# Kernel optimization log

Hardware: AMD Instinct MI355X
Metric: run time of the kernel (lower is better)

Reference implementation:

```python
import jax, jax.numpy as jnp
import numpy as np

B, S, D, H, F, L = 8, 1024, 512, 8, 2048, 2
SLOTS, OUT = 512, 32
NEG = jnp.finfo(jnp.float32).min


def _ln(x, scale, bias, eps=1e-6):
    mu = jnp.mean(x, axis=-1, keepdims=True)
    var = jnp.var(x, axis=-1, keepdims=True)
    return (x - mu) * jax.lax.rsqrt(var + eps) * scale + bias


def _mha(q_in, kv_in, Wq, Wk, Wv, Wo, mask):
    # flax MultiHeadDotProductAttention, use_bias=False; query scaled by 1/sqrt(head_dim)
    hd = D // H
    b = q_in.shape[0]
    q = (q_in @ Wq).reshape(b, -1, H, hd) / jnp.sqrt(jnp.float32(hd))
    k = (kv_in @ Wk).reshape(b, -1, H, hd)
    v = (kv_in @ Wv).reshape(b, -1, H, hd)
    scores = jnp.einsum('bqhd,bkhd->bhqk', q, k)
    scores = jnp.where(mask, scores, NEG)
    w = jax.nn.softmax(scores, axis=-1)
    o = jnp.einsum('bhqk,bkhd->bqhd', w, v).reshape(b, -1, D)
    return o @ Wo


def _forward(s, x, t, Wq, Wk, Wv, Wo, cWq, cWk, cWv, cWo, ln1_s, ln1_b, ln2_s, ln2_b, ln3_s, ln3_b, W1, b1, W2, b2, lnf_s, lnf_b, Wout, bout, W_vs, b_vs, W_ss, b_ss):
    causal = jnp.tril(jnp.ones((S, S), dtype=bool))[None, None]  # [1,1,S,S]
    eye = jnp.eye(S, dtype=bool)[None, None]                     # [1,1,S,S]
    dec = s
    for l in range(L):
        dec = _ln(dec + _mha(dec, dec, Wq[l], Wk[l], Wv[l], Wo[l], causal), ln1_s[l], ln1_b[l])
        dec = _ln(dec + _mha(dec, t, cWq[l], cWk[l], cWv[l], cWo[l], eye), ln2_s[l], ln2_b[l])
        ff = jax.nn.relu(dec @ W1[l] + b1[l]) @ W2[l] + b2[l]
        dec = _ln(dec + ff, ln3_s[l], ln3_b[l])
    logits = _ln(dec, lnf_s, lnf_b) @ Wout + bout  # [B,S,D]
    keys = jax.nn.softmax(logits.reshape(-1, logits.shape[-1]), axis=1)  # [N,D]
    Vs = (keys @ W_vs + b_vs).reshape(-1, SLOTS, OUT)  # [N,slots,out]
    Ss = keys @ W_ss + b_ss                            # [N,slots]
    xf = x.reshape(-1, OUT)                            # [N,out]
    denom = jnp.linalg.norm(Vs, axis=2) * jnp.linalg.norm(xf, axis=1, keepdims=True)  # [N,slots]
    scores = jnp.einsum('nko,no->nk', Vs, xf) / denom
    idx = jnp.argmax(scores, axis=1)  # [N]
    s_out = jnp.take_along_axis(Ss, idx[:, None], axis=1).reshape(-1, S)            # [B,S]
    v_out = jnp.take_along_axis(Vs, idx[:, None, None], axis=1).reshape(-1, S, OUT)  # [B,S,out]
    return v_out, s_out, Ss


def setup_inputs():
    key = jax.random.key(0)
    ks = iter(jax.random.split(key, 32))
    def r(shape, sc=0.02):
        return jax.random.normal(next(ks), shape, jnp.float32) * sc
    return {
        's': jax.random.normal(next(ks), (B, S, D), jnp.float32),
        'x': jax.random.normal(next(ks), (B, S, OUT), jnp.float32),
        't': jax.random.normal(next(ks), (B, S, D), jnp.float32),
        'Wq': r((L, D, D)), 'Wk': r((L, D, D)), 'Wv': r((L, D, D)), 'Wo': r((L, D, D)),
        'cWq': r((L, D, D)), 'cWk': r((L, D, D)), 'cWv': r((L, D, D)), 'cWo': r((L, D, D)),
        'ln1_s': jnp.ones((L, D)), 'ln1_b': jnp.zeros((L, D)),
        'ln2_s': jnp.ones((L, D)), 'ln2_b': jnp.zeros((L, D)),
        'ln3_s': jnp.ones((L, D)), 'ln3_b': jnp.zeros((L, D)),
        'W1': r((L, D, F)), 'b1': jnp.zeros((L, F)),
        'W2': r((L, F, D)), 'b2': jnp.zeros((L, D)),
        'lnf_s': jnp.ones((D,)), 'lnf_b': jnp.zeros((D,)),
        'Wout': r((D, D)), 'bout': jnp.zeros((D,)),
        'W_vs': r((D, SLOTS * OUT)), 'b_vs': jnp.zeros((SLOTS * OUT,)),
        'W_ss': r((D, SLOTS)), 'b_ss': jnp.zeros((SLOTS,)),
    }


def reference(s, x, t, Wq, Wk, Wv, Wo, cWq, cWk, cWv, cWo, ln1_s, ln1_b, ln2_s, ln2_b, ln3_s, ln3_b, W1, b1, W2, b2, lnf_s, lnf_b, Wout, bout, W_vs, b_vs, W_ss, b_ss):
    return _forward(s, x, t, Wq, Wk, Wv, Wo, cWq, cWk, cWv, cWo, ln1_s, ln1_b, ln2_s, ln2_b, ln3_s, ln3_b, W1, b1, W2, b2, lnf_s, lnf_b, Wout, bout, W_vs, b_vs, W_ss, b_ss)
```

## Files before the change

### kernel.cpp

```cpp
#include <hip/hip_runtime.h>
#include <math.h>

namespace {
constexpr int kD   = 512;
constexpr int kN   = 8192;
constexpr int kS   = 1024;
constexpr int kHD  = 64;
constexpr int kFF  = 2048;
constexpr int kSL  = 512;
constexpr int kOUT = 32;
}

typedef __bf16 bf16x8 __attribute__((ext_vector_type(8)));
typedef float  f32x4  __attribute__((ext_vector_type(4)));

__device__ inline unsigned short f2bf(float x) {
    unsigned u = __float_as_uint(x);
    return (unsigned short)((u + 0x7FFF + ((u >> 16) & 1)) >> 16);
}
__device__ inline void split2(float x, unsigned short& h, unsigned short& l) {
    unsigned u = __float_as_uint(x);
    unsigned hb = (u + 0x7FFF + ((u >> 16) & 1)) >> 16;
    h = (unsigned short)hb;
    float hf = __uint_as_float(hb << 16);
    l = f2bf(x - hf);
}

template<int MODE, int RELU, int HAS_BIAS>
__global__ __launch_bounds__(256)
void mgemm_k(const unsigned short* __restrict__ Ah, const unsigned short* __restrict__ Al,
             const unsigned short* __restrict__ Bh, const unsigned short* __restrict__ Bl,
             const float* __restrict__ bias, float* __restrict__ C,
             unsigned short* __restrict__ Ch, unsigned short* __restrict__ Cl,
             const float* __restrict__ X, const float* __restrict__ XN,
             float* __restrict__ SC,
             int M, int N, int K, float alpha)
{
    __shared__ uint4 smem_u4[4096];
    unsigned char* smem = (unsigned char*)smem_u4;
    const int tid  = threadIdx.x;
    const int lane = tid & 63;
    const int w    = tid >> 6;
    const int brow = blockIdx.y * 128;
    const int bcol = blockIdx.x * 128;
    const int wr = (w >> 1) * 64, wc = (w & 1) * 64;
    const size_t Kb = (size_t)K * 2;

    const unsigned short* srcM; int rb;
    if      (w == 0) { srcM = Ah; rb = brow; }
    else if (w == 1) { srcM = Al; rb = brow; }
    else if (w == 2) { srcM = Bh; rb = bcol; }
    else             { srcM = Bl; rb = bcol; }
    const int swzsrc = (((lane & 7) << 4) ^ (((lane >> 3) & 7) << 4));
    const unsigned char* srow = (const unsigned char*)srcM
                              + (size_t)(rb + (lane >> 3)) * Kb + swzsrc;
    unsigned char* dbase = smem + w * 16384;

    const int lm = lane & 15;
    const int lg = lane >> 4;
    const int lswz = (lane & 7);

    f32x4 acc[4][4];
#pragma unroll
    for (int i = 0; i < 4; ++i)
#pragma unroll
        for (int j = 0; j < 4; ++j) acc[i][j] = (f32x4)(0.f);

    for (int k0 = 0; k0 < K; k0 += 64) {
#pragma unroll
        for (int j = 0; j < 16; ++j) {
            const unsigned char* sp = srow + (size_t)(j * 8) * Kb + (size_t)k0 * 2;
            __builtin_amdgcn_global_load_lds(
                (const __attribute__((address_space(1))) unsigned int*)sp,
                (__attribute__((address_space(3))) unsigned int*)(dbase + j * 1024),
                16, 0, 0);
        }
        __syncthreads();
#pragma unroll
        for (int ks = 0; ks < 2; ++ks) {
            const int kf = (((ks << 2) + lg) ^ lswz) << 4;
            bf16x8 bh[4], bl[4];
#pragma unroll
            for (int n = 0; n < 4; ++n) {
                const int r = wc + n * 16 + lm;
                bh[n] = *(const bf16x8*)(smem + 32768 + r * 128 + kf);
                bl[n] = *(const bf16x8*)(smem + 49152 + r * 128 + kf);
            }
#pragma unroll
            for (int m = 0; m < 4; ++m) {
                const int r = wr + m * 16 + lm;
                bf16x8 ah = *(const bf16x8*)(smem +         r * 128 + kf);
                bf16x8 al = *(const bf16x8*)(smem + 16384 + r * 128 + kf);
#pragma unroll
                for (int n = 0; n < 4; ++n) {
                    acc[m][n] = __builtin_amdgcn_mfma_f32_16x16x32_bf16(al, bh[n], acc[m][n], 0, 0, 0);
                    acc[m][n] = __builtin_amdgcn_mfma_f32_16x16x32_bf16(ah, bl[n], acc[m][n], 0, 0, 0);
                    acc[m][n] = __builtin_amdgcn_mfma_f32_16x16x32_bf16(ah, bh[n], acc[m][n], 0, 0, 0);
                }
            }
        }
        __syncthreads();
    }

    if (MODE == 0 || MODE == 1) {
#pragma unroll
        for (int n = 0; n < 4; ++n) {
            const int colg = bcol + wc + n * 16 + lm;
            const float bv = HAS_BIAS ? bias[colg] : 0.f;
#pragma unroll
            for (int m = 0; m < 4; ++m) {
                const int rowb = brow + wr + m * 16 + lg * 4;
#pragma unroll
                for (int r = 0; r < 4; ++r) {
                    float v = alpha * acc[m][n][r] + bv;
                    if (RELU) v = fmaxf(v, 0.f);
                    if (MODE == 0) {
                        C[(size_t)(rowb + r) * N + colg] = v;
                    } else {
                        unsigned short h, l;
                        split2(v, h, l);
                        Ch[(size_t)(rowb + r) * N + colg] = h;
                        Cl[(size_t)(rowb + r) * N + colg] = l;
                    }
                }
            }
        }
    } else {
        float bv[4];
#pragma unroll
        for (int n = 0; n < 4; ++n) bv[n] = bias[bcol + wc + n * 16 + lm];
        const int slot0 = (bcol + wc) >> 5;
#pragma unroll
        for (int m = 0; m < 4; ++m) {
#pragma unroll
            for (int r = 0; r < 4; ++r) {
                const int row = brow + wr + m * 16 + lg * 4 + r;
                const float x0 = X[(size_t)row * kOUT + lm];
                const float x1 = X[(size_t)row * kOUT + 16 + lm];
                const float xn = XN[row];
#pragma unroll
                for (int s = 0; s < 2; ++s) {
                    const float v0 = acc[m][2 * s][r]     + bv[2 * s];
                    const float v1 = acc[m][2 * s + 1][r] + bv[2 * s + 1];
                    float pd = v0 * x0 + v1 * x1;
                    float pn = v0 * v0 + v1 * v1;
                    pd += __shfl_xor(pd, 1); pd += __shfl_xor(pd, 2);
                    pd += __shfl_xor(pd, 4); pd += __shfl_xor(pd, 8);
                    pn += __shfl_xor(pn, 1); pn += __shfl_xor(pn, 2);
                    pn += __shfl_xor(pn, 4); pn += __shfl_xor(pn, 8);
                    if (lm == 0)
                        SC[(size_t)row * kSL + slot0 + s] = pd / (sqrtf(pn) * xn);
                }
            }
        }
    }
}

__global__ __launch_bounds__(256)
void tsplit_k(const float* __restrict__ W, unsigned short* __restrict__ TH,
              unsigned short* __restrict__ TL, int K, int N)
{
    __shared__ float t[32][33];
    const int tid = threadIdx.x;
    const int n0 = blockIdx.x * 32, k0 = blockIdx.y * 32;
    {
        const int r = tid >> 3, c = (tid & 7) * 4;
        const float4 v = *(const float4*)(W + (size_t)(k0 + r) * N + n0 + c);
        t[r][c] = v.x; t[r][c + 1] = v.y; t[r][c + 2] = v.z; t[r][c + 3] = v.w;
    }
    __syncthreads();
    const int rn = tid >> 3, ck = (tid & 7) * 4;
    unsigned short h[4], l[4];
#pragma unroll
    for (int i = 0; i < 4; ++i) split2(t[ck + i][rn], h[i], l[i]);
    *(ushort4*)(TH + (size_t)(n0 + rn) * K + k0 + ck) = make_ushort4(h[0], h[1], h[2], h[3]);
    *(ushort4*)(TL + (size_t)(n0 + rn) * K + k0 + ck) = make_ushort4(l[0], l[1], l[2], l[3]);
}

__global__ __launch_bounds__(256)
void split_k(const float* __restrict__ in, unsigned short* __restrict__ hi,
             unsigned short* __restrict__ lo, int n4)
{
    int i = blockIdx.x * 256 + threadIdx.x;
    const int stride = gridDim.x * 256;
    for (; i < n4; i += stride) {
        const float4 v = *(const float4*)(in + (size_t)i * 4);
        unsigned short h[4], l[4];
        split2(v.x, h[0], l[0]); split2(v.y, h[1], l[1]);
        split2(v.z, h[2], l[2]); split2(v.w, h[3], l[3]);
        *(ushort4*)(hi + (size_t)i * 4) = make_ushort4(h[0], h[1], h[2], h[3]);
        *(ushort4*)(lo + (size_t)i * 4) = make_ushort4(l[0], l[1], l[2], l[3]);
    }
}

__global__ __launch_bounds__(256)
void attn_k(const float* __restrict__ Q, const float* __restrict__ K,
            const float* __restrict__ V, float* __restrict__ O)
{
    __shared__ float Qs[64][68];
    __shared__ float Ks[64][68];
    __shared__ float Vs[64][68];
    __shared__ float Ps[64][68];
    const int tid = threadIdx.x;
    const int tr = tid >> 4, tc = tid & 15;
    const int qt = blockIdx.x & 15;
    const int h  = (blockIdx.x >> 4) & 7;
    const int b  = blockIdx.x >> 7;
    const int q0 = qt * 64;
    const float* Qb = Q + ((size_t)(b * kS + q0)) * kD + h * kHD;
    {
        const int r = tid >> 2;
#pragma unroll
        for (int it = 0; it < 4; ++it) {
            const int e0 = ((tid & 3) << 2) + it * 16;
            const float4 q4 = *(const float4*)(Qb + (size_t)r * kD + e0);
            Qs[e0 + 0][r] = q4.x; Qs[e0 + 1][r] = q4.y;
            Qs[e0 + 2][r] = q4.z; Qs[e0 + 3][r] = q4.w;
        }
    }
    float m[4], l[4], acc[4][4];
#pragma unroll
    for (int i = 0; i < 4; ++i) {
        m[i] = -INFINITY; l[i] = 0.f;
#pragma unroll
        for (int j = 0; j < 4; ++j) acc[i][j] = 0.f;
    }
    for (int j0 = 0; j0 <= q0; j0 += 64) {
        const float* Kb = K + ((size_t)(b * kS + j0)) * kD + h * kHD;
        const float* Vb = V + ((size_t)(b * kS + j0)) * kD + h * kHD;
        __syncthreads();
        {
            const int c = tid >> 2;
#pragma unroll
            for (int it = 0; it < 4; ++it) {
                const int e0 = ((tid & 3) << 2) + it * 16;
                const float4 k4 = *(const float4*)(Kb + (size_t)c * kD + e0);
                Ks[e0 + 0][c] = k4.x; Ks[e0 + 1][c] = k4.y;
                Ks[e0 + 2][c] = k4.z; Ks[e0 + 3][c] = k4.w;
                *(float4*)&Vs[c][e0] = *(const float4*)(Vb + (size_t)c * kD + e0);
            }
        }
        __syncthreads();
        float s[4][4];
#pragma unroll
        for (int i = 0; i < 4; ++i)
#pragma unroll
            for (int j = 0; j < 4; ++j) s[i][j] = 0.f;
        for (int e = 0; e < 64; ++e) {
            float qa[4], kb[4];
            *(float4*)&qa[0] = *(const float4*)&Qs[e][tr * 4];
            *(float4*)&kb[0] = *(const float4*)&Ks[e][tc * 4];
#pragma unroll
            for (int i = 0; i < 4; ++i)
#pragma unroll
                for (int j = 0; j < 4; ++j)
                    s[i][j] = fmaf(qa[i], kb[j], s[i][j]);
        }
        if (j0 == q0) {
#pragma unroll
            for (int i = 0; i < 4; ++i)
#pragma unroll
                for (int j = 0; j < 4; ++j)
                    if (tc * 4 + j > tr * 4 + i) s[i][j] = -INFINITY;
        }
#pragma unroll
        for (int i = 0; i < 4; ++i) {
            float rm = fmaxf(fmaxf(s[i][0], s[i][1]), fmaxf(s[i][2], s[i][3]));
            rm = fmaxf(rm, __shfl_xor(rm, 1));
            rm = fmaxf(rm, __shfl_xor(rm, 2));
            rm = fmaxf(rm, __shfl_xor(rm, 4));
            rm = fmaxf(rm, __shfl_xor(rm, 8));
            const float mn = fmaxf(m[i], rm);
            const float co = expf(m[i] - mn);
            float ps = 0.f;
#pragma unroll
            for (int j = 0; j < 4; ++j) { s[i][j] = expf(s[i][j] - mn); ps += s[i][j]; }
            ps += __shfl_xor(ps, 1); ps += __shfl_xor(ps, 2);
            ps += __shfl_xor(ps, 4); ps += __shfl_xor(ps, 8);
            l[i] = l[i] * co + ps;
            m[i] = mn;
#pragma unroll
            for (int j = 0; j < 4; ++j) acc[i][j] *= co;
            *(float4*)&Ps[tr * 4 + i][tc * 4] = make_float4(s[i][0], s[i][1], s[i][2], s[i][3]);
        }
        __syncthreads();
        for (int c = 0; c < 64; ++c) {
            const float4 v4 = *(const float4*)&Vs[c][tc * 4];
#pragma unroll
            for (int i = 0; i < 4; ++i) {
                const float p = Ps[tr * 4 + i][c];
                acc[i][0] = fmaf(p, v4.x, acc[i][0]);
                acc[i][1] = fmaf(p, v4.y, acc[i][1]);
                acc[i][2] = fmaf(p, v4.z, acc[i][2]);
                acc[i][3] = fmaf(p, v4.w, acc[i][3]);
            }
        }
    }
    float* Ob = O + ((size_t)(b * kS + q0)) * kD + h * kHD;
#pragma unroll
    for (int i = 0; i < 4; ++i) {
        const float inv = 1.0f / l[i];
        *(float4*)(Ob + (size_t)(tr * 4 + i) * kD + tc * 4) =
            make_float4(acc[i][0] * inv, acc[i][1] * inv, acc[i][2] * inv, acc[i][3] * inv);
    }
}

__global__ __launch_bounds__(256)
void ln_k(const float* __restrict__ a, const float* __restrict__ b,
          const float* __restrict__ sc, const float* __restrict__ bi,
          float* __restrict__ out, unsigned short* __restrict__ oh,
          unsigned short* __restrict__ ol)
{
    const int w = threadIdx.x >> 6, lane = threadIdx.x & 63;
    const size_t row = (size_t)blockIdx.x * 4 + w;
    const float* ap = a + row * kD;
    float x[8];
    *(float4*)&x[0] = *(const float4*)(ap + lane * 8);
    *(float4*)&x[4] = *(const float4*)(ap + lane * 8 + 4);
    if (b) {
        const float* bp = b + row * kD;
        float y[8];
        *(float4*)&y[0] = *(const float4*)(bp + lane * 8);
        *(float4*)&y[4] = *(const float4*)(bp + lane * 8 + 4);
#pragma unroll
        for (int k = 0; k < 8; ++k) x[k] += y[k];
    }
    float s = 0.f;
#pragma unroll
    for (int k = 0; k < 8; ++k) s += x[k];
    for (int msk = 1; msk < 64; msk <<= 1) s += __shfl_xor(s, msk);
    const float mean = s * (1.0f / 512.0f);
    float v = 0.f;
#pragma unroll
    for (int k = 0; k < 8; ++k) { const float d = x[k] - mean; v = fmaf(d, d, v); }
    for (int msk = 1; msk < 64; msk <<= 1) v += __shfl_xor(v, msk);
    const float rstd = 1.0f / sqrtf(v * (1.0f / 512.0f) + 1e-6f);
    float o[8]; unsigned short h[8], lo2[8];
#pragma unroll
    for (int k = 0; k < 8; ++k) {
        const int col = lane * 8 + k;
        o[k] = (x[k] - mean) * rstd * sc[col] + bi[col];
        split2(o[k], h[k], lo2[k]);
    }
    *(float4*)(out + row * kD + lane * 8)     = *(const float4*)&o[0];
    *(float4*)(out + row * kD + lane * 8 + 4) = *(const float4*)&o[4];
    *(ushort4*)(oh + row * kD + lane * 8)     = make_ushort4(h[0], h[1], h[2], h[3]);
    *(ushort4*)(oh + row * kD + lane * 8 + 4) = make_ushort4(h[4], h[5], h[6], h[7]);
    *(ushort4*)(ol + row * kD + lane * 8)     = make_ushort4(lo2[0], lo2[1], lo2[2], lo2[3]);
    *(ushort4*)(ol + row * kD + lane * 8 + 4) = make_ushort4(lo2[4], lo2[5], lo2[6], lo2[7]);
}

__global__ __launch_bounds__(256)
void softmax_k(const float* __restrict__ in, float* __restrict__ out,
               unsigned short* __restrict__ oh, unsigned short* __restrict__ ol)
{
    const int w = threadIdx.x >> 6, lane = threadIdx.x & 63;
    const size_t row = (size_t)blockIdx.x * 4 + w;
    const float* ip = in + row * kD;
    float x[8];
    *(float4*)&x[0] = *(const float4*)(ip + lane * 8);
    *(float4*)&x[4] = *(const float4*)(ip + lane * 8 + 4);
    float mx = x[0];
#pragma unroll
    for (int k = 1; k < 8; ++k) mx = fmaxf(mx, x[k]);
    for (int msk = 1; msk < 64; msk <<= 1) mx = fmaxf(mx, __shfl_xor(mx, msk));
    float s = 0.f;
#pragma unroll
    for (int k = 0; k < 8; ++k) { x[k] = expf(x[k] - mx); s += x[k]; }
    for (int msk = 1; msk < 64; msk <<= 1) s += __shfl_xor(s, msk);
    const float inv = 1.0f / s;
    unsigned short h[8], lo2[8];
#pragma unroll
    for (int k = 0; k < 8; ++k) { x[k] *= inv; split2(x[k], h[k], lo2[k]); }
    *(float4*)(out + row * kD + lane * 8)     = *(const float4*)&x[0];
    *(float4*)(out + row * kD + lane * 8 + 4) = *(const float4*)&x[4];
    *(ushort4*)(oh + row * kD + lane * 8)     = make_ushort4(h[0], h[1], h[2], h[3]);
    *(ushort4*)(oh + row * kD + lane * 8 + 4) = make_ushort4(h[4], h[5], h[6], h[7]);
    *(ushort4*)(ol + row * kD + lane * 8)     = make_ushort4(lo2[0], lo2[1], lo2[2], lo2[3]);
    *(ushort4*)(ol + row * kD + lane * 8 + 4) = make_ushort4(lo2[4], lo2[5], lo2[6], lo2[7]);
}

__global__ __launch_bounds__(256)
void xnorm_k(const float* __restrict__ X, float* __restrict__ XN)
{
    const int tid = threadIdx.x;
    const int row = blockIdx.x * 8 + (tid >> 5);
    const int o = tid & 31;
    const float v = X[(size_t)row * kOUT + o];
    float s = v * v;
    s += __shfl_xor(s, 1); s += __shfl_xor(s, 2); s += __shfl_xor(s, 4);
    s += __shfl_xor(s, 8); s += __shfl_xor(s, 16);
    if (o == 0) XN[row] = sqrtf(s);
}

__global__ __launch_bounds__(256)
void pick_k(const float* __restrict__ scores, const float* __restrict__ keys,
            const float* __restrict__ Wvs, const float* __restrict__ bvs,
            const float* __restrict__ Ss, float* __restrict__ vout,
            float* __restrict__ sout)
{
    const int n = blockIdx.x;
    const int tid = threadIdx.x;
    __shared__ float sv[256];
    __shared__ int   si[256];
    __shared__ float ks[512];
    __shared__ float red[256];
    const float s0 = scores[(size_t)n * kSL + tid];
    const float s1 = scores[(size_t)n * kSL + tid + 256];
    float bs; int bi;
    if (s1 > s0) { bs = s1; bi = tid + 256; } else { bs = s0; bi = tid; }
    sv[tid] = bs; si[tid] = bi;
    ks[tid] = keys[(size_t)n * kD + tid];
    ks[tid + 256] = keys[(size_t)n * kD + tid + 256];
    __syncthreads();
    for (int off = 128; off > 0; off >>= 1) {
        if (tid < off) {
            const float ov = sv[tid + off]; const int oi = si[tid + off];
            if (ov > sv[tid] || (ov == sv[tid] && oi < si[tid])) { sv[tid] = ov; si[tid] = oi; }
        }
        __syncthreads();
    }
    const int idx = si[0];
    const int o = tid & 31;
    const int seg = tid >> 5;
    const float* Wc = Wvs + (size_t)idx * kOUT + o;
    float part = 0.f;
    for (int d = seg * 64; d < seg * 64 + 64; ++d)
        part = fmaf(ks[d], Wc[(size_t)d * (kSL * kOUT)], part);
    red[tid] = part;
    __syncthreads();
    if (tid < 32) {
        float t = red[tid];
#pragma unroll
        for (int ss = 1; ss < 8; ++ss) t += red[tid + 32 * ss];
        vout[(size_t)n * kOUT + tid] = t + bvs[idx * kOUT + tid];
    }
    if (tid == 0) sout[n] = Ss[(size_t)n * kSL + idx];
}

extern "C" void kernel_launch(void* const* d_in, const int* in_sizes, int n_in,
                              void* d_out, int out_size, void* d_ws, size_t ws_size,
                              hipStream_t stream)
{
    (void)in_sizes; (void)n_in; (void)out_size; (void)ws_size;
    const float* s_in = (const float*)d_in[0];
    const float* x_in = (const float*)d_in[1];
    const float* t_in = (const float*)d_in[2];
    const float* Wq   = (const float*)d_in[3];
    const float* Wk   = (const float*)d_in[4];
    const float* Wv   = (const float*)d_in[5];
    const float* Wo   = (const float*)d_in[6];
    const float* cWv  = (const float*)d_in[9];
    const float* cWo  = (const float*)d_in[10];
    const float* ln1s = (const float*)d_in[11];
    const float* ln1b = (const float*)d_in[12];
    const float* ln2s = (const float*)d_in[13];
    const float* ln2b = (const float*)d_in[14];
    const float* ln3s = (const float*)d_in[15];
    const float* ln3b = (const float*)d_in[16];
    const float* W1   = (const float*)d_in[17];
    const float* b1   = (const float*)d_in[18];
    const float* W2   = (const float*)d_in[19];
    const float* b2   = (const float*)d_in[20];
    const float* lnfs = (const float*)d_in[21];
    const float* lnfb = (const float*)d_in[22];
    const float* Wout = (const float*)d_in[23];
    const float* bout = (const float*)d_in[24];
    const float* Wvs  = (const float*)d_in[25];
    const float* bvs  = (const float*)d_in[26];
    const float* Wss  = (const float*)d_in[27];
    const float* bss  = (const float*)d_in[28];

    float* out_v  = (float*)d_out;
    float* out_s  = out_v + (size_t)kN * kOUT;
    float* out_Ss = out_s + kN;

    unsigned char* w8 = (unsigned char*)d_ws;
    const size_t MD = (size_t)kN * kD;
    float* f_dec = (float*)w8;
    float* f_A   = f_dec + MD;
    float* f_B   = f_A + MD;
    float* f_C   = f_B + MD;
    float* f_xn  = f_C + MD;
    unsigned short* dH = (unsigned short*)(f_xn + kN);
    unsigned short* dL = dH + MD;
    unsigned short* hH = dL + MD;
    unsigned short* hL = hH + (size_t)kN * kFF;
    unsigned short* wTH = hL + (size_t)kN * kFF;
    unsigned short* wTL = wTH + (size_t)kSL * kOUT * kD;
    unsigned short* sH = hH;
    unsigned short* sL = hL;
    unsigned short* kH = hH + MD;
    unsigned short* kL = hL + MD;

    const dim3 blk(256);
    const size_t DD = (size_t)kD * kD;

    auto tsplit = [&](const float* W, int K, int N) {
        tsplit_k<<<dim3(N / 32, K / 32), blk, 0, stream>>>(W, wTH, wTL, K, N);
    };
    auto gemm = [&](const unsigned short* aH, const unsigned short* aL,
                    const float* bias, float* out, int N, int K, float alpha) {
        if (bias)
            mgemm_k<0, 0, 1><<<dim3(N / 128, kN / 128), blk, 0, stream>>>(
                aH, aL, wTH, wTL, bias, out, nullptr, nullptr, nullptr, nullptr, nullptr,
                kN, N, K, alpha);
        else
            mgemm_k<0, 0, 0><<<dim3(N / 128, kN / 128), blk, 0, stream>>>(
                aH, aL, wTH, wTL, nullptr, out, nullptr, nullptr, nullptr, nullptr, nullptr,
                kN, N, K, alpha);
    };

    xnorm_k<<<kN / 8, blk, 0, stream>>>(x_in, f_xn);
    split_k<<<1024, blk, 0, stream>>>(s_in, dH, dL, (int)(MD / 4));

    const float* cur = s_in;
    for (int l = 0; l < 2; ++l) {
        const size_t wo = (size_t)l * DD;
        tsplit(Wq + wo, kD, kD); gemm(dH, dL, nullptr, f_A, kD, kD, 0.125f);
        tsplit(Wk + wo, kD, kD); gemm(dH, dL, nullptr, f_B, kD, kD, 1.f);
        tsplit(Wv + wo, kD, kD); gemm(dH, dL, nullptr, f_C, kD, kD, 1.f);
        attn_k<<<1024, blk, 0, stream>>>(f_A, f_B, f_C, f_A);
        split_k<<<1024, blk, 0, stream>>>(f_A, sH, sL, (int)(MD / 4));
        tsplit(Wo + wo, kD, kD); gemm(sH, sL, nullptr, f_B, kD, kD, 1.f);
        ln_k<<<kN / 4, blk, 0, stream>>>(cur, f_B, ln1s + l * kD, ln1b + l * kD, f_dec, dH, dL);
        split_k<<<1024, blk, 0, stream>>>(t_in, sH, sL, (int)(MD / 4));
        tsplit(cWv + wo, kD, kD); gemm(sH, sL, nullptr, f_A, kD, kD, 1.f);
        split_k<<<1024, blk, 0, stream>>>(f_A, sH, sL, (int)(MD / 4));
        tsplit(cWo + wo, kD, kD); gemm(sH, sL, nullptr, f_A, kD, kD, 1.f);
        ln_k<<<kN / 4, blk, 0, stream>>>(f_dec, f_A, ln2s + l * kD, ln2b + l * kD, f_dec, dH, dL);
        tsplit(W1 + (size_t)l * kD * kFF, kD, kFF);
        mgemm_k<1, 1, 1><<<dim3(kFF / 128, kN / 128), blk, 0, stream>>>(
            dH, dL, wTH, wTL, b1 + (size_t)l * kFF, nullptr, hH, hL,
            nullptr, nullptr, nullptr, kN, kFF, kD, 1.f);
        tsplit(W2 + (size_t)l * kFF * kD, kFF, kD);
        gemm(hH, hL, b2 + (size_t)l * kD, f_A, kD, kFF, 1.f);
        ln_k<<<kN / 4, blk, 0, stream>>>(f_dec, f_A, ln3s + l * kD, ln3b + l * kD, f_dec, dH, dL);
        cur = f_dec;
    }
    ln_k<<<kN / 4, blk, 0, stream>>>(f_dec, nullptr, lnfs, lnfb, f_A, dH, dL);
    tsplit(Wout, kD, kD); gemm(dH, dL, bout, f_B, kD, kD, 1.f);
    softmax_k<<<kN / 4, blk, 0, stream>>>(f_B, f_A, kH, kL);
    tsplit(Wss, kD, kSL); gemm(kH, kL, bss, out_Ss, kSL, kD, 1.f);
    tsplit(Wvs, kD, kSL * kOUT);
    mgemm_k<2, 0, 1><<<dim3(kSL * kOUT / 128, kN / 128), blk, 0, stream>>>(
        kH, kL, wTH, wTL, bvs, nullptr, nullptr, nullptr, x_in, f_xn, f_C,
        kN, kSL * kOUT, kD, 1.f);
    pick_k<<<kN, blk, 0, stream>>>(f_C, f_A, Wvs, bvs, out_Ss, out_v, out_s);
}
```

Baseline: 2.190 ms.

## Add double-buffered 256x256 split-bf16 GEMM for the large FFN and slot GEMMs

Adds a new GEMM kernel with 256x256 output tiles and 512 threads. It double-buffers LDS across K-steps of 32, using async global-to-LDS loads overlapped with MFMA compute through explicit vmcnt waits. It also remaps block IDs so that nearby blocks are spread across groups of eight. The W1 FFN GEMM and the large N=16384 slot-value GEMM with the fused cosine-score epilogue use it, which should cut per-tile load traffic and hide load latency. The smaller 128-tile kernel keeps its old loop, gains the same block remap, and drops its unused epilogue arguments. The larger tiles raise register pressure and use 128KB of LDS per block, which may limit occupancy.

```diff
diff --git a/kernel.cpp b/kernel.cpp
--- a/kernel.cpp
+++ b/kernel.cpp
@@ -27,79 +27,88 @@
 }
 
 template<int MODE, int RELU, int HAS_BIAS>
-__global__ __launch_bounds__(256)
-void mgemm_k(const unsigned short* __restrict__ Ah, const unsigned short* __restrict__ Al,
-             const unsigned short* __restrict__ Bh, const unsigned short* __restrict__ Bl,
-             const float* __restrict__ bias, float* __restrict__ C,
-             unsigned short* __restrict__ Ch, unsigned short* __restrict__ Cl,
-             const float* __restrict__ X, const float* __restrict__ XN,
-             float* __restrict__ SC,
-             int M, int N, int K, float alpha)
-{
-    __shared__ uint4 smem_u4[4096];
-    unsigned char* smem = (unsigned char*)smem_u4;
-    const int tid  = threadIdx.x;
-    const int lane = tid & 63;
-    const int w    = tid >> 6;
-    const int brow = blockIdx.y * 128;
-    const int bcol = blockIdx.x * 128;
-    const int wr = (w >> 1) * 64, wc = (w & 1) * 64;
-    const size_t Kb = (size_t)K * 2;
-
-    const unsigned short* srcM; int rb;
-    if      (w == 0) { srcM = Ah; rb = brow; }
-    else if (w == 1) { srcM = Al; rb = brow; }
-    else if (w == 2) { srcM = Bh; rb = bcol; }
-    else             { srcM = Bl; rb = bcol; }
-    const int swzsrc = (((lane & 7) << 4) ^ (((lane >> 3) & 7) << 4));
-    const unsigned char* srow = (const unsigned char*)srcM
-                              + (size_t)(rb + (lane >> 3)) * Kb + swzsrc;
-    unsigned char* dbase = smem + w * 16384;
-
-    const int lm = lane & 15;
-    const int lg = lane >> 4;
-    const int lswz = (lane & 7);
-
-    f32x4 acc[4][4];
-#pragma unroll
-    for (int i = 0; i < 4; ++i)
+__global__ __launch_bounds__(512, 2)
+void mgemm256_k(const unsigned short* __restrict__ Ah, const unsigned short* __restrict__ Al,
+                const unsigned short* __restrict__ Bh, const unsigned short* __restrict__ Bl,
+                const float* __restrict__ bias, float* __restrict__ C,
+                unsigned short* __restrict__ Ch, unsigned short* __restrict__ Cl,
+                const float* __restrict__ X, const float* __restrict__ XN,
+                float* __restrict__ SC,
+                int M, int N, int K, float alpha)
+{
+    __shared__ uint4 smem4[8192];
+    unsigned char* smem = (unsigned char*)smem4;
+    const int tid = threadIdx.x, lane = tid & 63, w = tid >> 6;
+
+    const int gx = gridDim.x;
+    int bid = blockIdx.y * gx + blockIdx.x;
+    const int nwg = gx * gridDim.y;
+    bid = (bid & 7) * (nwg >> 3) + (bid >> 3);
+    const int bx = bid % gx, by = bid / gx;
+    const int brow = by * 256, bcol = bx * 256;
+    const int wr = (w >> 2) * 128, wc = (w & 3) * 64;
+    const size_t K2 = (size_t)K * 2;
+
+    const int p = w >> 1, hf = w & 1;
+    const unsigned short* SP = (p == 0) ? Ah : (p == 1) ? Al : (p == 2) ? Bh : Bl;
+    const int rbase = (p < 2) ? brow : bcol;
+    const int cch = ((lane & 3) - ((lane >> 3) & 3)) & 3;
+    const unsigned char* src0 = (const unsigned char*)SP
+        + (size_t)(rbase + hf * 128 + (lane >> 2)) * K2 + (cch << 4);
+    const int ldsw0 = (p << 14) + (hf << 13);
+
+    const int lm = lane & 15, lg = lane >> 4;
+    const int sw = ((lg + (lm >> 1)) & 3) << 4;
+    const int aoff = (wr + lm) * 64 + sw;
+    const int boff = 32768 + (wc + lm) * 64 + sw;
+
+    f32x4 acc[8][4];
+#pragma unroll
+    for (int i = 0; i < 8; ++i)
 #pragma unroll
         for (int j = 0; j < 4; ++j) acc[i][j] = (f32x4)(0.f);
 
-    for (int k0 = 0; k0 < K; k0 += 64) {
-#pragma unroll
-        for (int j = 0; j < 16; ++j) {
-            const unsigned char* sp = srow + (size_t)(j * 8) * Kb + (size_t)k0 * 2;
+    auto stage = [&](int bufo_, int t_) {
+        const unsigned char* s_ = src0 + (size_t)t_ * 64;
+#pragma unroll
+        for (int j = 0; j < 8; ++j)
             __builtin_amdgcn_global_load_lds(
-                (const __attribute__((address_space(1))) unsigned int*)sp,
-                (__attribute__((address_space(3))) unsigned int*)(dbase + j * 1024),
+                (const __attribute__((address_space(1))) unsigned int*)(s_ + (size_t)j * 16 * K2),
+                (__attribute__((address_space(3))) unsigned int*)(smem + bufo_ + ldsw0 + j * 1024),
                 16, 0, 0);
-        }
-        __syncthreads();
-#pragma unroll
-        for (int ks = 0; ks < 2; ++ks) {
-            const int kf = (((ks << 2) + lg) ^ lswz) << 4;
-            bf16x8 bh[4], bl[4];
+    };
+
+    const int nt = K >> 5;
+    stage(0, 0);
+    for (int t = 0; t < nt; ++t) {
+        if (t + 1 < nt) {
+            stage(((t + 1) & 1) << 16, t + 1);
+            asm volatile("s_waitcnt vmcnt(8)" ::: "memory");
+        } else {
+            asm volatile("s_waitcnt vmcnt(0)" ::: "memory");
+        }
+        __builtin_amdgcn_s_barrier();
+        __builtin_amdgcn_sched_barrier(0);
+        const unsigned char* base = smem + ((t & 1) << 16);
+        bf16x8 bh[4], bl[4];
+#pragma unroll
+        for (int n = 0; n < 4; ++n) {
+            bh[n] = *(const bf16x8*)(base + boff + n * 1024);
+            bl[n] = *(const bf16x8*)(base + boff + 16384 + n * 1024);
+        }
+#pragma unroll
+        for (int m = 0; m < 8; ++m) {
+            bf16x8 ah = *(const bf16x8*)(base + aoff + m * 1024);
+            bf16x8 al = *(const bf16x8*)(base + aoff + 16384 + m * 1024);
 #pragma unroll
             for (int n = 0; n < 4; ++n) {
-                const int r = wc + n * 16 + lm;
-                bh[n] = *(const bf16x8*)(smem + 32768 + r * 128 + kf);
-                bl[n] = *(const bf16x8*)(smem + 49152 + r * 128 + kf);
-            }
-#pragma unroll
-            for (int m = 0; m < 4; ++m) {
-                const int r = wr + m * 16 + lm;
-                bf16x8 ah = *(const bf16x8*)(smem +         r * 128 + kf);
-                bf16x8 al = *(const bf16x8*)(smem + 16384 + r * 128 + kf);
-#pragma unroll
-                for (int n = 0; n < 4; ++n) {
-                    acc[m][n] = __builtin_amdgcn_mfma_f32_16x16x32_bf16(al, bh[n], acc[m][n], 0, 0, 0);
-                    acc[m][n] = __builtin_amdgcn_mfma_f32_16x16x32_bf16(ah, bl[n], acc[m][n], 0, 0, 0);
-                    acc[m][n] = __builtin_amdgcn_mfma_f32_16x16x32_bf16(ah, bh[n], acc[m][n], 0, 0, 0);
-                }
-            }
-        }
-        __syncthreads();
+                acc[m][n] = __builtin_amdgcn_mfma_f32_16x16x32_bf16(al, bh[n], acc[m][n], 0, 0, 0);
+                acc[m][n] = __builtin_amdgcn_mfma_f32_16x16x32_bf16(ah, bl[n], acc[m][n], 0, 0, 0);
+                acc[m][n] = __builtin_amdgcn_mfma_f32_16x16x32_bf16(ah, bh[n], acc[m][n], 0, 0, 0);
+            }
+        }
+        __builtin_amdgcn_sched_barrier(0);
+        __builtin_amdgcn_s_barrier();
     }
 
     if (MODE == 0 || MODE == 1) {
@@ -108,7 +117,7 @@
             const int colg = bcol + wc + n * 16 + lm;
             const float bv = HAS_BIAS ? bias[colg] : 0.f;
 #pragma unroll
-            for (int m = 0; m < 4; ++m) {
+            for (int m = 0; m < 8; ++m) {
                 const int rowb = brow + wr + m * 16 + lg * 4;
 #pragma unroll
                 for (int r = 0; r < 4; ++r) {
@@ -131,7 +140,7 @@
         for (int n = 0; n < 4; ++n) bv[n] = bias[bcol + wc + n * 16 + lm];
         const int slot0 = (bcol + wc) >> 5;
 #pragma unroll
-        for (int m = 0; m < 4; ++m) {
+        for (int m = 0; m < 8; ++m) {
 #pragma unroll
             for (int r = 0; r < 4; ++r) {
                 const int row = brow + wr + m * 16 + lg * 4 + r;
@@ -150,6 +159,109 @@
                     pn += __shfl_xor(pn, 4); pn += __shfl_xor(pn, 8);
                     if (lm == 0)
                         SC[(size_t)row * kSL + slot0 + s] = pd / (sqrtf(pn) * xn);
+                }
+            }
+        }
+    }
+}
+
+template<int MODE, int RELU, int HAS_BIAS>
+__global__ __launch_bounds__(256)
+void mgemm_k(const unsigned short* __restrict__ Ah, const unsigned short* __restrict__ Al,
+             const unsigned short* __restrict__ Bh, const unsigned short* __restrict__ Bl,
+             const float* __restrict__ bias, float* __restrict__ C,
+             unsigned short* __restrict__ Ch, unsigned short* __restrict__ Cl,
+             int M, int N, int K, float alpha)
+{
+    __shared__ uint4 smem_u4[4096];
+    unsigned char* smem = (unsigned char*)smem_u4;
+    const int tid  = threadIdx.x;
+    const int lane = tid & 63;
+    const int w    = tid >> 6;
+    const int gx = gridDim.x;
+    int bid = blockIdx.y * gx + blockIdx.x;
+    const int nwg = gx * gridDim.y;
+    bid = (bid & 7) * (nwg >> 3) + (bid >> 3);
+    const int bxs = bid % gx, bys = bid / gx;
+    const int brow = bys * 128;
+    const int bcol = bxs * 128;
+    const int wr = (w >> 1) * 64, wc = (w & 1) * 64;
+    const size_t Kb = (size_t)K * 2;
+
+    const unsigned short* srcM; int rb;
+    if      (w == 0) { srcM = Ah; rb = brow; }
+    else if (w == 1) { srcM = Al; rb = brow; }
+    else if (w == 2) { srcM = Bh; rb = bcol; }
+    else             { srcM = Bl; rb = bcol; }
+    const int swzsrc = (((lane & 7) << 4) ^ (((lane >> 3) & 7) << 4));
+    const unsigned char* srow = (const unsigned char*)srcM
+                              + (size_t)(rb + (lane >> 3)) * Kb + swzsrc;
+    unsigned char* dbase = smem + w * 16384;
+
+    const int lm = lane & 15;
+    const int lg = lane >> 4;
+    const int lswz = (lane & 7);
+
+    f32x4 acc[4][4];
+#pragma unroll
+    for (int i = 0; i < 4; ++i)
+#pragma unroll
+        for (int j = 0; j < 4; ++j) acc[i][j] = (f32x4)(0.f);
+
+    for (int k0 = 0; k0 < K; k0 += 64) {
+#pragma unroll
+        for (int j = 0; j < 16; ++j) {
+            const unsigned char* sp = srow + (size_t)(j * 8) * Kb + (size_t)k0 * 2;
+            __builtin_amdgcn_global_load_lds(
+                (const __attribute__((address_space(1))) unsigned int*)sp,
+                (__attribute__((address_space(3))) unsigned int*)(dbase + j * 1024),
+                16, 0, 0);
+        }
+        __syncthreads();
+#pragma unroll
+        for (int ks = 0; ks < 2; ++ks) {
+            const int kf = (((ks << 2) + lg) ^ lswz) << 4;
+            bf16x8 bh[4], bl[4];
+#pragma unroll
+            for (int n = 0; n < 4; ++n) {
+                const int r = wc + n * 16 + lm;
+                bh[n] = *(const bf16x8*)(smem + 32768 + r * 128 + kf);
+                bl[n] = *(const bf16x8*)(smem + 49152 + r * 128 + kf);
+            }
+#pragma unroll
+            for (int m = 0; m < 4; ++m) {
+                const int r = wr + m * 16 + lm;
+                bf16x8 ah = *(const bf16x8*)(smem +         r * 128 + kf);
+                bf16x8 al = *(const bf16x8*)(smem + 16384 + r * 128 + kf);
+#pragma unroll
+                for (int n = 0; n < 4; ++n) {
+                    acc[m][n] = __builtin_amdgcn_mfma_f32_16x16x32_bf16(al, bh[n], acc[m][n], 0, 0, 0);
+                    acc[m][n] = __builtin_amdgcn_mfma_f32_16x16x32_bf16(ah, bl[n], acc[m][n], 0, 0, 0);
+                    acc[m][n] = __builtin_amdgcn_mfma_f32_16x16x32_bf16(ah, bh[n], acc[m][n], 0, 0, 0);
+                }
+            }
+        }
+        __syncthreads();
+    }
+
+#pragma unroll
+    for (int n = 0; n < 4; ++n) {
+        const int colg = bcol + wc + n * 16 + lm;
+        const float bv = HAS_BIAS ? bias[colg] : 0.f;
+#pragma unroll
+        for (int m = 0; m < 4; ++m) {
+            const int rowb = brow + wr + m * 16 + lg * 4;
+#pragma unroll
+            for (int r = 0; r < 4; ++r) {
+                float v = alpha * acc[m][n][r] + bv;
+                if (RELU) v = fmaxf(v, 0.f);
+                if (MODE == 0) {
+                    C[(size_t)(rowb + r) * N + colg] = v;
+                } else {
+                    unsigned short h, l;
+                    split2(v, h, l);
+                    Ch[(size_t)(rowb + r) * N + colg] = h;
+                    Cl[(size_t)(rowb + r) * N + colg] = l;
                 }
             }
         }
@@ -494,6 +606,7 @@
     unsigned short* kL = hL + MD;
 
     const dim3 blk(256);
+    const dim3 blk512(512);
     const size_t DD = (size_t)kD * kD;
 
     auto tsplit = [&](const float* W, int K, int N) {
@@ -503,12 +616,10 @@
                     const float* bias, float* out, int N, int K, float alpha) {
         if (bias)
             mgemm_k<0, 0, 1><<<dim3(N / 128, kN / 128), blk, 0, stream>>>(
-                aH, aL, wTH, wTL, bias, out, nullptr, nullptr, nullptr, nullptr, nullptr,
-                kN, N, K, alpha);
+                aH, aL, wTH, wTL, bias, out, nullptr, nullptr, kN, N, K, alpha);
         else
             mgemm_k<0, 0, 0><<<dim3(N / 128, kN / 128), blk, 0, stream>>>(
-                aH, aL, wTH, wTL, nullptr, out, nullptr, nullptr, nullptr, nullptr, nullptr,
-                kN, N, K, alpha);
+                aH, aL, wTH, wTL, nullptr, out, nullptr, nullptr, kN, N, K, alpha);
     };
 
     xnorm_k<<<kN / 8, blk, 0, stream>>>(x_in, f_xn);
@@ -530,7 +641,7 @@
         tsplit(cWo + wo, kD, kD); gemm(sH, sL, nullptr, f_A, kD, kD, 1.f);
         ln_k<<<kN / 4, blk, 0, stream>>>(f_dec, f_A, ln2s + l * kD, ln2b + l * kD, f_dec, dH, dL);
         tsplit(W1 + (size_t)l * kD * kFF, kD, kFF);
-        mgemm_k<1, 1, 1><<<dim3(kFF / 128, kN / 128), blk, 0, stream>>>(
+        mgemm256_k<1, 1, 1><<<dim3(kFF / 256, kN / 256), blk512, 0, stream>>>(
             dH, dL, wTH, wTL, b1 + (size_t)l * kFF, nullptr, hH, hL,
             nullptr, nullptr, nullptr, kN, kFF, kD, 1.f);
         tsplit(W2 + (size_t)l * kFF * kD, kFF, kD);
@@ -543,7 +654,7 @@
     softmax_k<<<kN / 4, blk, 0, stream>>>(f_B, f_A, kH, kL);
     tsplit(Wss, kD, kSL); gemm(kH, kL, bss, out_Ss, kSL, kD, 1.f);
     tsplit(Wvs, kD, kSL * kOUT);
-    mgemm_k<2, 0, 1><<<dim3(kSL * kOUT / 128, kN / 128), blk, 0, stream>>>(
+    mgemm256_k<2, 0, 1><<<dim3(kSL * kOUT / 256, kN / 256), blk512, 0, stream>>>(
         kH, kL, wTH, wTL, bvs, nullptr, nullptr, nullptr, x_in, f_xn, f_C,
         kN, kSL * kOUT, kD, 1.f);
     pick_k<<<kN, blk, 0, stream>>>(f_C, f_A, Wvs, bvs, out_Ss, out_v, out_s);
```

After: 2.119 ms. 1.03x faster.
